# Kernel optimization log

Hardware: AMD Instinct MI355X
Metric: run time of the kernel (lower is better)

The kernel has to match this reference:

```python
import jax, jax.numpy as jnp
import numpy as np

D_MODEL = 1024
NUM_HEADS = 16
D_K = D_MODEL // NUM_HEADS
THETA = 10000.0
B, S = 4, 2048


def _rope(x, theta=THETA):
    # x: [b, n, s, d_k]; interleaved pair rotation with base theta
    d = x.shape[-1]
    s = x.shape[-2]
    inv_freq = theta ** (-jnp.arange(0, d, 2, dtype=jnp.float32) / d)  # [d/2]
    pos = jnp.arange(s, dtype=jnp.float32)
    ang = pos[:, None] * inv_freq[None, :]          # [s, d/2]
    cos, sin = jnp.cos(ang), jnp.sin(ang)           # broadcast over b, n
    x1 = x[..., 0::2]
    x2 = x[..., 1::2]
    r1 = x1 * cos - x2 * sin
    r2 = x1 * sin + x2 * cos
    out = jnp.stack([r1, r2], axis=-1).reshape(x.shape)
    return out.astype(x.dtype)


def setup_inputs() -> dict:
    key = jax.random.key(0)
    ks = jax.random.split(key, 5)
    scale = 1.0 / np.sqrt(D_MODEL)
    return {
        "x": jax.random.normal(ks[0], (B, S, D_MODEL), dtype=jnp.float32),
        "W_q": jax.random.normal(ks[1], (D_MODEL, D_MODEL), dtype=jnp.float32) * scale,
        "W_k": jax.random.normal(ks[2], (D_MODEL, D_MODEL), dtype=jnp.float32) * scale,
        "W_v": jax.random.normal(ks[3], (D_MODEL, D_MODEL), dtype=jnp.float32) * scale,
        "W_o": jax.random.normal(ks[4], (D_MODEL, D_MODEL), dtype=jnp.float32) * scale,
    }


def reference(x, W_q, W_k, W_v, W_o):
    b, s, _ = x.shape
    # QKV projections (Linear stores weight as [out, in]; y = x @ W.T)
    q = jnp.einsum("bsd,ed->bse", x, W_q).reshape(b, s, NUM_HEADS, D_K).transpose(0, 2, 1, 3)
    k = jnp.einsum("bsd,ed->bse", x, W_k).reshape(b, s, NUM_HEADS, D_K).transpose(0, 2, 1, 3)
    v = jnp.einsum("bsd,ed->bse", x, W_v).reshape(b, s, NUM_HEADS, D_K).transpose(0, 2, 1, 3)
    q = _rope(q)
    k = _rope(k)
    scale = 1.0 / jnp.sqrt(jnp.asarray(D_K, dtype=x.dtype))
    scores = jnp.einsum("bnqd,bnkd->bnqk", q, k) * scale  # [b,n,s,s]
    causal = jnp.tril(jnp.ones((s, s), dtype=bool))
    scores = jnp.where(causal, scores, jnp.asarray(-jnp.inf, dtype=scores.dtype))
    attn = jax.nn.softmax(scores, axis=-1)
    out = jnp.einsum("bnqk,bnkd->bnqd", attn, v)          # [b,n,s,d_k]
    out = out.transpose(0, 2, 1, 3).reshape(b, s, D_MODEL)
    return jnp.einsum("bsd,ed->bse", out, W_o)
```

## Files before the change

### kernel.cpp

```cpp
#include <hip/hip_runtime.h>

#define AS1 __attribute__((address_space(1)))
#define AS3 __attribute__((address_space(3)))

typedef short short8 __attribute__((ext_vector_type(8)));
typedef float f32x4 __attribute__((ext_vector_type(4)));

#define DM 1024
#define NH 16
#define DKH 64
#define SEQ 2048
#define NB 4
#define ROWS (NB*SEQ)
#define QTILES (SEQ/128)

__device__ __forceinline__ unsigned short f2bf(float x) {
    union { float f; unsigned u; } v; v.f = x;
    unsigned r = v.u + 0x7fffu + ((v.u >> 16) & 1u);
    return (unsigned short)(r >> 16);
}
__device__ __forceinline__ float bf2f(unsigned short b) {
    union { unsigned u; float f; } v; v.u = ((unsigned)b) << 16;
    return v.f;
}
__device__ __forceinline__ unsigned cvtpk_bf16(float lo, float hi) {
    unsigned r;
    asm("v_cvt_pk_bf16_f32 %0, %1, %2" : "=v"(r) : "v"(lo), "v"(hi));
    return r;
}

__device__ __forceinline__ void gload_lds16(const void* g, void* l) {
    const AS1 unsigned int* gp = (const AS1 unsigned int*)(unsigned long long)g;
    AS3 unsigned int* lp = (AS3 unsigned int*)(unsigned)(unsigned long long)l;
    __builtin_amdgcn_global_load_lds(gp, lp, 16, 0, 0);
}

__device__ __forceinline__ f32x4 mfma_bf16(short8 a, short8 b, f32x4 c) {
    return __builtin_amdgcn_mfma_f32_16x16x32_bf16(a, b, c, 0, 0, 0);
}

__global__ void __launch_bounds__(256) prep_kernel(
    const float* __restrict__ x,
    const float* __restrict__ Wq, const float* __restrict__ Wk,
    const float* __restrict__ Wv, const float* __restrict__ Wo,
    unsigned short* __restrict__ xb, unsigned short* __restrict__ wbase,
    float2* __restrict__ tab) {
    int bid = blockIdx.x, tid = threadIdx.x;
    if (bid < 12288) {
        const float* src;
        unsigned short* dst;
        int i;
        if (bid < 8192) {
            src = x; dst = xb; i = bid * 256 + tid;
        } else {
            int id2 = bid - 8192;
            int w = id2 >> 10;
            src = w == 0 ? Wq : (w == 1 ? Wk : (w == 2 ? Wv : Wo));
            dst = wbase + (size_t)w * (1024 * 1024);
            i = (id2 & 1023) * 256 + tid;
        }
        float4 v = reinterpret_cast<const float4*>(src)[i];
        ushort4 o;
        o.x = f2bf(v.x); o.y = f2bf(v.y); o.z = f2bf(v.z); o.w = f2bf(v.w);
        reinterpret_cast<ushort4*>(dst)[i] = o;
    } else {
        int idx = (bid - 12288) * 256 + tid;
        int pos = idx >> 5, i = idx & 31;
        float inv = powf(10000.0f, -(float)i * (1.0f / 32.0f));
        float ang = (float)pos * inv;
        float2 cs; cs.x = cosf(ang); cs.y = sinf(ang);
        tab[idx] = cs;
    }
}

template <int STORE_F32>
__device__ __forceinline__ void gemm_bt_body(const unsigned short* __restrict__ A,
                                             const unsigned short* __restrict__ Bw,
                                             void* __restrict__ C, int m0, int n0,
                                             const float2* __restrict__ tab, float rs,
                                             unsigned short* __restrict__ vt, int outmode) {
    __shared__ unsigned short S[128 * 128];
    unsigned short* As = S;
    unsigned short* Bs = S + 128 * 64;
    const int tid = threadIdx.x;
    const int lane = tid & 63;
    const int wave = tid >> 6;
    const int wr = wave >> 1, wc = wave & 1;
    const int l15 = lane & 15, l4 = lane >> 4;

    f32x4 acc[4][4];
    #pragma unroll
    for (int m = 0; m < 4; ++m)
        #pragma unroll
        for (int n = 0; n < 4; ++n) { f32x4 z = {0.f, 0.f, 0.f, 0.f}; acc[m][n] = z; }

    const int srow = wave * 8 + (lane >> 3);
    const int gsw = (lane & 7) ^ (srow & 7);
    const unsigned short* Ag = A + (size_t)m0 * DM;
    const unsigned short* Bg = Bw + (size_t)n0 * DM;

    for (int kt = 0; kt < DM; kt += 64) {
        __syncthreads();
        #pragma unroll
        for (int it = 0; it < 4; ++it) {
            int row = it * 32 + srow;
            gload_lds16(Ag + (size_t)row * DM + kt + gsw * 8, (char*)As + (it * 4 + wave) * 1024);
            gload_lds16(Bg + (size_t)row * DM + kt + gsw * 8, (char*)Bs + (it * 4 + wave) * 1024);
        }
        __syncthreads();
        #pragma unroll
        for (int kc = 0; kc < 2; ++kc) {
            short8 af[4], bfr[4];
            #pragma unroll
            for (int m = 0; m < 4; ++m) {
                int row = 64 * wr + 16 * m + l15;
                int off = row * 128 + (((4 * kc + l4) ^ (row & 7)) << 4);
                af[m] = *(const short8*)((const char*)As + off);
            }
            #pragma unroll
            for (int n = 0; n < 4; ++n) {
                int row = 64 * wc + 16 * n + l15;
                int off = row * 128 + (((4 * kc + l4) ^ (row & 7)) << 4);
                bfr[n] = *(const short8*)((const char*)Bs + off);
            }
            #pragma unroll
            for (int m = 0; m < 4; ++m)
                #pragma unroll
                for (int n = 0; n < 4; ++n)
                    acc[m][n] = mfma_bf16(af[m], bfr[n], acc[m][n]);
        }
    }

    if (STORE_F32) {
        int rbase = m0 + 64 * wr + 4 * l4;
        int cbase = n0 + 64 * wc + l15;
        #pragma unroll
        for (int m = 0; m < 4; ++m)
            #pragma unroll
            for (int n = 0; n < 4; ++n) {
                int c = cbase + 16 * n;
                #pragma unroll
                for (int j = 0; j < 4; ++j)
                    ((float*)C)[(size_t)(rbase + 16 * m + j) * DM + c] = acc[m][n][j];
            }
    } else {
        __syncthreads();
        #pragma unroll
        for (int m = 0; m < 4; ++m) {
            int rb = 64 * wr + 16 * m + 4 * l4;
            int xr = ((rb >> 2) & 7) << 3;
            #pragma unroll
            for (int n = 0; n < 4; ++n) {
                int c = (64 * wc + 16 * n + l15) ^ xr;
                #pragma unroll
                for (int j = 0; j < 4; ++j)
                    S[(rb + j) * 128 + c] = f2bf(acc[m][n][j]);
            }
        }
        __syncthreads();
        if (outmode == 2) {
            int bidx = m0 >> 11;
            int stile = m0 & (SEQ - 1);
            int hA = n0 >> 6;
            unsigned short* vtb = vt + (size_t)(bidx * (NH * 64) + hA * 64) * SEQ;
            #pragma unroll
            for (int rep = 0; rep < 8; ++rep) {
                int idx = rep * 256 + tid;
                int vtrow = idx >> 4;
                int grp = idx & 15;
                int tg = grp >> 3, kg = grp & 7;
                int kc = kg >> 2, mq = kg & 3;
                short8 o;
                #pragma unroll
                for (int jj = 0; jj < 8; ++jj) {
                    int t = 32 * kc + 16 * (jj >> 2) + 4 * mq + (jj & 3);
                    int r = tg * 64 + t;
                    o[jj] = (short)S[r * 128 + (vtrow ^ (((r >> 2) & 7) << 3))];
                }
                *(short8*)(vtb + (size_t)vtrow * SEQ + stile + tg * 64 + kg * 8) = o;
            }
        } else {
            unsigned short* Cg = (unsigned short*)C + (size_t)m0 * DM + n0;
            #pragma unroll
            for (int r8 = 0; r8 < 8; ++r8) {
                int row = r8 * 16 + (tid >> 4);
                int oc = tid & 15;
                short8 v = *(const short8*)(S + row * 128 + ((oc ^ ((row >> 2) & 7)) << 3));
                if (rs > 0.f) {
                    int pos = (m0 + row) & (SEQ - 1);
                    const float2* tp = tab + pos * 32 + (oc & 7) * 4;
                    short8 o;
                    #pragma unroll
                    for (int tt = 0; tt < 4; ++tt) {
                        float cc = tp[tt].x * rs, ss = tp[tt].y * rs;
                        float e0 = bf2f((unsigned short)v[2 * tt]);
                        float e1 = bf2f((unsigned short)v[2 * tt + 1]);
                        o[2 * tt]     = (short)f2bf(e0 * cc - e1 * ss);
                        o[2 * tt + 1] = (short)f2bf(e0 * ss + e1 * cc);
                    }
                    v = o;
                }
                *(short8*)(Cg + (size_t)row * DM + oc * 8) = v;
            }
        }
    }
}

__global__ void __launch_bounds__(256) gemm_qkv_kernel(
    const unsigned short* __restrict__ X,
    const unsigned short* __restrict__ Wq, const unsigned short* __restrict__ Wk,
    const unsigned short* __restrict__ Wv,
    unsigned short* __restrict__ Qo, unsigned short* __restrict__ Ko,
    unsigned short* __restrict__ Vtg,
    const float2* __restrict__ tab) {
    const float CS = 0.125f * 1.44269504088896f;
    int mt = blockIdx.x >> 3, nt = blockIdx.x & 7;
    int z = blockIdx.z;
    const unsigned short* W = z == 0 ? Wq : (z == 1 ? Wk : Wv);
    unsigned short* O = z == 0 ? Qo : Ko;
    gemm_bt_body<0>(X, W, O, mt * 128, nt * 128, tab,
                    z == 0 ? CS : (z == 1 ? 1.0f : 0.f), Vtg, z == 2 ? 2 : 0);
}

__global__ void __launch_bounds__(256) gemm_out_kernel(
    const unsigned short* __restrict__ AO, const unsigned short* __restrict__ Wo,
    float* __restrict__ out) {
    int mt = blockIdx.x >> 3, nt = blockIdx.x & 7;
    gemm_bt_body<1>(AO, Wo, out, mt * 128, nt * 128, nullptr, 0.f, nullptr, 0);
}

template <int MODE>
__device__ __forceinline__ void attn_tile(const char* bK, const char* bV,
                                          const short8 (&aq)[2][2], f32x4 (&oacc)[2][4],
                                          float (&lrow)[2],
                                          int l15, int l4, int qloc) {
    f32x4 sac[2][4];
    #pragma unroll
    for (int f = 0; f < 2; ++f)
        #pragma unroll
        for (int n = 0; n < 4; ++n) { f32x4 z = {0.f, 0.f, 0.f, 0.f}; sac[f][n] = z; }

    #pragma unroll
    for (int kc = 0; kc < 2; ++kc)
        #pragma unroll
        for (int n = 0; n < 4; ++n) {
            int row = 16 * n + l15;
            short8 ak = *(const short8*)(bK + row * 128 + (((4 * kc + l4) ^ (row & 7)) << 4));
            if (MODE < 2) sac[0][n] = mfma_bf16(ak, aq[0][kc], sac[0][n]);
            sac[1][n] = mfma_bf16(ak, aq[1][kc], sac[1][n]);
        }

    short8 pb[2][2];
    #pragma unroll
    for (int f = (MODE == 2 ? 1 : 0); f < 2; ++f) {
        const bool dg = (MODE == 1 && f == 0) || (MODE == 2);
        float pj[4][4];
        float sum = 0.f;
        #pragma unroll
        for (int n = 0; n < 4; ++n)
            #pragma unroll
            for (int j = 0; j < 4; ++j) {
                float s = sac[f][n][j];
                if (dg && (16 * n + 4 * l4 + j) > qloc) s = -1e30f;
                float p = exp2f(s);
                pj[n][j] = p; sum += p;
            }
        sum += __shfl_xor(sum, 16, 64);
        sum += __shfl_xor(sum, 32, 64);
        lrow[f] += sum;
        #pragma unroll
        for (int kc = 0; kc < 2; ++kc) {
            union { unsigned u[4]; short8 s8; } P;
            P.u[0] = cvtpk_bf16(pj[2 * kc][0], pj[2 * kc][1]);
            P.u[1] = cvtpk_bf16(pj[2 * kc][2], pj[2 * kc][3]);
            P.u[2] = cvtpk_bf16(pj[2 * kc + 1][0], pj[2 * kc + 1][1]);
            P.u[3] = cvtpk_bf16(pj[2 * kc + 1][2], pj[2 * kc + 1][3]);
            pb[f][kc] = P.s8;
        }
    }

    #pragma unroll
    for (int kc = 0; kc < 2; ++kc)
        #pragma unroll
        for (int n = 0; n < 4; ++n) {
            int row = 16 * n + l15;
            short8 av = *(const short8*)(bV + row * 128 + (((4 * kc + l4) ^ (row & 7)) << 4));
            if (MODE < 2) oacc[0][n] = mfma_bf16(av, pb[0][kc], oacc[0][n]);
            oacc[1][n] = mfma_bf16(av, pb[1][kc], oacc[1][n]);
        }
}

__global__ void __launch_bounds__(256) attn_kernel(const unsigned short* __restrict__ Q,
                                                   const unsigned short* __restrict__ K,
                                                   const unsigned short* __restrict__ Vtg,
                                                   unsigned short* __restrict__ O) {
    __shared__ unsigned short smem[16384];

    const int tid = threadIdx.x, lane = tid & 63, wave = tid >> 6;
    const int l15 = lane & 15, l4 = lane >> 4;
    const int bh = blockIdx.x;
    const int yg = blockIdx.y >> 2, yl = blockIdx.y & 3;
    const int qt = yg == 0 ? 15 - yl : (yg == 1 ? yl : (yg == 2 ? 11 - yl : 4 + yl));
    const int b = bh >> 4, h = bh & 15;
    const size_t base = (size_t)b * SEQ * DM + (size_t)h * DKH;
    const unsigned short* Qb = Q + base;
    const unsigned short* Kb = K + base;
    const unsigned short* Vg = Vtg + (size_t)bh * 64 * SEQ;
    unsigned short* Ob = O + base;

    const int q0 = qt * 128;
    const int qloc = 16 * wave + l15;
    const int NT = 2 * qt + 2;

    short8 aq[2][2];
    #pragma unroll
    for (int f = 0; f < 2; ++f) {
        const unsigned short* p = Qb + (size_t)(q0 + 64 * f + 16 * wave + l15) * DM + 8 * l4;
        aq[f][0] = *(const short8*)p;
        aq[f][1] = *(const short8*)(p + 32);
    }
    asm volatile("s_waitcnt vmcnt(0)" ::: "memory");

    f32x4 oacc[2][4];
    #pragma unroll
    for (int f = 0; f < 2; ++f)
        #pragma unroll
        for (int n = 0; n < 4; ++n) { f32x4 z = {0.f, 0.f, 0.f, 0.f}; oacc[f][n] = z; }
    float lrow[2] = {0.f, 0.f};

    const int srow = wave * 8 + (lane >> 3);
    const int gsw = (lane & 7) ^ (srow & 7);
    const unsigned short* kp = Kb + (size_t)srow * DM + gsw * 8;
    const unsigned short* vp = Vg + (size_t)srow * SEQ + gsw * 8;
    char* LD = (char*)smem;

    {
        char* db = LD;
        gload_lds16(kp, db + wave * 1024);
        gload_lds16(kp + 32 * DM, db + 4096 + wave * 1024);
        gload_lds16(vp, db + 8192 + wave * 1024);
        gload_lds16(vp + 32 * SEQ, db + 12288 + wave * 1024);
        kp += 64 * DM; vp += 64;
    }

    for (int t = 0; t < NT; ++t) {
        const char* bK = LD + (t & 1) * 16384;
        const char* bV = bK + 8192;
        if (t + 1 < NT) {
            char* db = LD + ((t + 1) & 1) * 16384;
            gload_lds16(kp, db + wave * 1024);
            gload_lds16(kp + 32 * DM, db + 4096 + wave * 1024);
            gload_lds16(vp, db + 8192 + wave * 1024);
            gload_lds16(vp + 32 * SEQ, db + 12288 + wave * 1024);
            kp += 64 * DM; vp += 64;
            asm volatile("s_waitcnt vmcnt(4)" ::: "memory");
        } else {
            asm volatile("s_waitcnt vmcnt(0)" ::: "memory");
        }
        __builtin_amdgcn_s_barrier();
        if (t < NT - 2)       attn_tile<0>(bK, bV, aq, oacc, lrow, l15, l4, qloc);
        else if (t == NT - 2) attn_tile<1>(bK, bV, aq, oacc, lrow, l15, l4, qloc);
        else                  attn_tile<2>(bK, bV, aq, oacc, lrow, l15, l4, qloc);
        asm volatile("s_waitcnt lgkmcnt(0)" ::: "memory");
        __builtin_amdgcn_s_barrier();
    }

    unsigned short* ep = smem + wave * 2304;
    float inv[2] = {1.f / lrow[0], 1.f / lrow[1]};
    #pragma unroll
    for (int f = 0; f < 2; ++f)
        #pragma unroll
        for (int n = 0; n < 4; ++n)
            #pragma unroll
            for (int j = 0; j < 4; ++j)
                ep[(f * 16 + l15) * 72 + 16 * n + 4 * l4 + j] = f2bf(oacc[f][n][j] * inv[f]);
    __syncthreads();
    #pragma unroll
    for (int i = 0; i < 4; ++i) {
        int r = i * 8 + (lane >> 3), cg = lane & 7;
        int grow = q0 + 64 * (r >> 4) + 16 * wave + (r & 15);
        *(short8*)(Ob + (size_t)grow * DM + cg * 8) = *(const short8*)(ep + r * 72 + cg * 8);
    }
}

extern "C" void kernel_launch(void* const* d_in, const int* in_sizes, int n_in,
                              void* d_out, int out_size, void* d_ws, size_t ws_size,
                              hipStream_t stream) {
    (void)in_sizes; (void)n_in; (void)out_size; (void)ws_size;
    const float* x  = (const float*)d_in[0];
    const float* Wq = (const float*)d_in[1];
    const float* Wk = (const float*)d_in[2];
    const float* Wv = (const float*)d_in[3];
    const float* Wo = (const float*)d_in[4];
    float* out = (float*)d_out;

    char* ws = (char*)d_ws;
    const size_t MB = 1024 * 1024;
    unsigned short* xb  = (unsigned short*)(ws);
    unsigned short* wqb = (unsigned short*)(ws + 16 * MB);
    unsigned short* wkb = (unsigned short*)(ws + 18 * MB);
    unsigned short* wvb = (unsigned short*)(ws + 20 * MB);
    unsigned short* wob = (unsigned short*)(ws + 22 * MB);
    unsigned short* Qb  = (unsigned short*)(ws + 24 * MB);
    unsigned short* Kb  = (unsigned short*)(ws + 40 * MB);
    unsigned short* Vtg = (unsigned short*)(ws + 56 * MB);
    unsigned short* AO  = (unsigned short*)(ws + 72 * MB);
    float2* tab = (float2*)(ws + 88 * MB);

    prep_kernel<<<12544, 256, 0, stream>>>(x, Wq, Wk, Wv, Wo, xb, wqb, tab);
    gemm_qkv_kernel<<<dim3(512, 1, 3), 256, 0, stream>>>(xb, wqb, wkb, wvb, Qb, Kb, Vtg, tab);
    attn_kernel<<<dim3(NB * NH, QTILES), 256, 0, stream>>>(Qb, Kb, Vtg, AO);
    gemm_out_kernel<<<512, 256, 0, stream>>>(AO, wob, out);
}
```

Measured before the change: 183.4 us.

## Add online-softmax max tracking and register-staged single-buffer K/V loads

Moves the softmax scale out of the Q projection into the attention tile and adds a running row max with rescaling of the accumulators and row sums. This is the standard numerically safe online softmax, replacing the unshifted exp2. The K/V prefetch changes from asynchronous global-to-LDS double buffering to loading into registers and storing into one LDS buffer after each tile. That halves LDS use but adds an extra barrier per iteration plus the max reduction, shuffles and rescale work.

Result: slower. 215.0 us (+17.3%).

```diff
diff --git a/kernel.cpp b/kernel.cpp
--- a/kernel.cpp
+++ b/kernel.cpp
@@ -213,13 +213,12 @@
     unsigned short* __restrict__ Qo, unsigned short* __restrict__ Ko,
     unsigned short* __restrict__ Vtg,
     const float2* __restrict__ tab) {
-    const float CS = 0.125f * 1.44269504088896f;
     int mt = blockIdx.x >> 3, nt = blockIdx.x & 7;
     int z = blockIdx.z;
     const unsigned short* W = z == 0 ? Wq : (z == 1 ? Wk : Wv);
     unsigned short* O = z == 0 ? Qo : Ko;
     gemm_bt_body<0>(X, W, O, mt * 128, nt * 128, tab,
-                    z == 0 ? CS : (z == 1 ? 1.0f : 0.f), Vtg, z == 2 ? 2 : 0);
+                    z < 2 ? 1.0f : 0.f, Vtg, z == 2 ? 2 : 0);
 }
 
 __global__ void __launch_bounds__(256) gemm_out_kernel(
@@ -230,10 +229,13 @@
 }
 
 template <int MODE>
-__device__ __forceinline__ void attn_tile(const char* bK, const char* bV,
+__device__ __forceinline__ void attn_tile(const unsigned short* bufKV,
                                           const short8 (&aq)[2][2], f32x4 (&oacc)[2][4],
-                                          float (&lrow)[2],
+                                          float (&mrow)[2], float (&lrow)[2],
                                           int l15, int l4, int qloc) {
+    const float CS = 0.125f * 1.44269504088896f;
+    const char* bK = (const char*)bufKV;
+    const char* bV = (const char*)bufKV + 8192;
     f32x4 sac[2][4];
     #pragma unroll
     for (int f = 0; f < 2; ++f)
@@ -254,20 +256,36 @@
     #pragma unroll
     for (int f = (MODE == 2 ? 1 : 0); f < 2; ++f) {
         const bool dg = (MODE == 1 && f == 0) || (MODE == 2);
+        float sv[4][4];
+        float tm = -1e30f;
+        #pragma unroll
+        for (int n = 0; n < 4; ++n)
+            #pragma unroll
+            for (int j = 0; j < 4; ++j) {
+                float s = sac[f][n][j] * CS;
+                if (dg && (16 * n + 4 * l4 + j) > qloc) s = -1e30f;
+                sv[n][j] = s;
+                tm = fmaxf(tm, s);
+            }
+        tm = fmaxf(tm, __shfl_xor(tm, 16, 64));
+        tm = fmaxf(tm, __shfl_xor(tm, 32, 64));
+        float nm = fmaxf(mrow[f], tm);
+        float al = exp2f(mrow[f] - nm);
+        mrow[f] = nm;
         float pj[4][4];
         float sum = 0.f;
         #pragma unroll
         for (int n = 0; n < 4; ++n)
             #pragma unroll
             for (int j = 0; j < 4; ++j) {
-                float s = sac[f][n][j];
-                if (dg && (16 * n + 4 * l4 + j) > qloc) s = -1e30f;
-                float p = exp2f(s);
+                float p = exp2f(sv[n][j] - nm);
                 pj[n][j] = p; sum += p;
             }
         sum += __shfl_xor(sum, 16, 64);
         sum += __shfl_xor(sum, 32, 64);
-        lrow[f] += sum;
+        lrow[f] = lrow[f] * al + sum;
+        #pragma unroll
+        for (int n = 0; n < 4; ++n) oacc[f][n] *= al;
         #pragma unroll
         for (int kc = 0; kc < 2; ++kc) {
             union { unsigned u[4]; short8 s8; } P;
@@ -294,7 +312,7 @@
                                                    const unsigned short* __restrict__ K,
                                                    const unsigned short* __restrict__ Vtg,
                                                    unsigned short* __restrict__ O) {
-    __shared__ unsigned short smem[16384];
+    __shared__ unsigned short smem[9216];
 
     const int tid = threadIdx.x, lane = tid & 63, wave = tid >> 6;
     const int l15 = lane & 15, l4 = lane >> 4;
@@ -319,50 +337,50 @@
         aq[f][0] = *(const short8*)p;
         aq[f][1] = *(const short8*)(p + 32);
     }
-    asm volatile("s_waitcnt vmcnt(0)" ::: "memory");
 
     f32x4 oacc[2][4];
     #pragma unroll
     for (int f = 0; f < 2; ++f)
         #pragma unroll
         for (int n = 0; n < 4; ++n) { f32x4 z = {0.f, 0.f, 0.f, 0.f}; oacc[f][n] = z; }
+    float mrow[2] = {-1e30f, -1e30f};
     float lrow[2] = {0.f, 0.f};
 
     const int srow = wave * 8 + (lane >> 3);
     const int gsw = (lane & 7) ^ (srow & 7);
     const unsigned short* kp = Kb + (size_t)srow * DM + gsw * 8;
     const unsigned short* vp = Vg + (size_t)srow * SEQ + gsw * 8;
-    char* LD = (char*)smem;
-
-    {
-        char* db = LD;
-        gload_lds16(kp, db + wave * 1024);
-        gload_lds16(kp + 32 * DM, db + 4096 + wave * 1024);
-        gload_lds16(vp, db + 8192 + wave * 1024);
-        gload_lds16(vp + 32 * SEQ, db + 12288 + wave * 1024);
-        kp += 64 * DM; vp += 64;
-    }
+    unsigned short* s0 = smem + ((0 * 4 + wave) * 1024 + lane * 16) / 2;
+    unsigned short* s1 = smem + ((1 * 4 + wave) * 1024 + lane * 16) / 2;
+    unsigned short* s2 = smem + (8192 + (0 * 4 + wave) * 1024 + lane * 16) / 2;
+    unsigned short* s3 = smem + (8192 + (1 * 4 + wave) * 1024 + lane * 16) / 2;
+
+    short8 rk0 = *(const short8*)(kp);
+    short8 rk1 = *(const short8*)(kp + 32 * DM);
+    short8 rv0 = *(const short8*)(vp);
+    short8 rv1 = *(const short8*)(vp + 32 * SEQ);
+    kp += 64 * DM; vp += 64;
+    *(short8*)s0 = rk0; *(short8*)s1 = rk1;
+    *(short8*)s2 = rv0; *(short8*)s3 = rv1;
+    __syncthreads();
 
     for (int t = 0; t < NT; ++t) {
-        const char* bK = LD + (t & 1) * 16384;
-        const char* bV = bK + 8192;
         if (t + 1 < NT) {
-            char* db = LD + ((t + 1) & 1) * 16384;
-            gload_lds16(kp, db + wave * 1024);
-            gload_lds16(kp + 32 * DM, db + 4096 + wave * 1024);
-            gload_lds16(vp, db + 8192 + wave * 1024);
-            gload_lds16(vp + 32 * SEQ, db + 12288 + wave * 1024);
+            rk0 = *(const short8*)(kp);
+            rk1 = *(const short8*)(kp + 32 * DM);
+            rv0 = *(const short8*)(vp);
+            rv1 = *(const short8*)(vp + 32 * SEQ);
             kp += 64 * DM; vp += 64;
-            asm volatile("s_waitcnt vmcnt(4)" ::: "memory");
-        } else {
-            asm volatile("s_waitcnt vmcnt(0)" ::: "memory");
-        }
-        __builtin_amdgcn_s_barrier();
-        if (t < NT - 2)       attn_tile<0>(bK, bV, aq, oacc, lrow, l15, l4, qloc);
-        else if (t == NT - 2) attn_tile<1>(bK, bV, aq, oacc, lrow, l15, l4, qloc);
-        else                  attn_tile<2>(bK, bV, aq, oacc, lrow, l15, l4, qloc);
-        asm volatile("s_waitcnt lgkmcnt(0)" ::: "memory");
-        __builtin_amdgcn_s_barrier();
+        }
+        if (t < NT - 2)       attn_tile<0>(smem, aq, oacc, mrow, lrow, l15, l4, qloc);
+        else if (t == NT - 2) attn_tile<1>(smem, aq, oacc, mrow, lrow, l15, l4, qloc);
+        else                  attn_tile<2>(smem, aq, oacc, mrow, lrow, l15, l4, qloc);
+        __syncthreads();
+        if (t + 1 < NT) {
+            *(short8*)s0 = rk0; *(short8*)s1 = rk1;
+            *(short8*)s2 = rv0; *(short8*)s3 = rv1;
+            __syncthreads();
+        }
     }
 
     unsigned short* ep = smem + wave * 2304;
```
